# Optimization experiments

Hardware: AMD Instinct MI355X
Metric: run time of the kernel (lower is better)

Reference implementation:

```python
import jax, jax.numpy as jnp
import numpy as np

N = 100_000      # num_nodes
E = 1_600_000    # num_edges (avg degree 16)
D = 64           # embedding_dim
L = 3            # num_layers


def setup_inputs() -> dict:
    key = jax.random.key(0)
    k1, k2 = jax.random.split(key)
    edge_index = jax.random.randint(k1, (2, E), 0, N, dtype=jnp.int64)
    edge_weight = jnp.ones((E,), jnp.float32)
    # nn.init.normal_(std=0.1)
    embedding = 0.1 * jax.random.normal(k2, (N, D), dtype=jnp.float32)
    return {"embedding": embedding, "edge_weight": edge_weight, "edge_index": edge_index}


def reference(embedding, edge_weight, edge_index):
    n = embedding.shape[0]
    self_idx = jnp.arange(n, dtype=edge_index.dtype)
    # add_self_loops: append (i, i) with weight 1 (PyG default fill_value)
    row = jnp.concatenate([edge_index[0], self_idx])  # source j
    col = jnp.concatenate([edge_index[1], self_idx])  # target i
    ew = jnp.concatenate([edge_weight, jnp.ones((n,), embedding.dtype)])
    # degree() counts occurrences of row (unweighted)
    deg = jax.ops.segment_sum(jnp.ones_like(ew), row, num_segments=n)
    deg_inv_sqrt = jnp.where(deg > 0, jax.lax.rsqrt(deg), 0.0)
    norm = deg_inv_sqrt[row] * ew * deg_inv_sqrt[col]  # [E+N]

    x = embedding
    acc = embedding  # running sum of layer-0..L embeddings
    for _ in range(L):
        # gather from source, scale, scatter-add to target (dropout off in eval)
        msg = norm[:, None] * x[row]                       # [E+N, D]
        x = jax.ops.segment_sum(msg, col, num_segments=n)  # [N, D]
        acc = acc + x
    return acc / (L + 1)
```

## Files before the change

kernel.cpp:

```cpp
#include <hip/hip_runtime.h>
#include <stdint.h>

#define DIM 64
#define GB 256
#define GSH 8
#define CH 4096
#define TB1 256
#define HW 25000
#define NSL 256
#define TBH 1024

__device__ __forceinline__ unsigned bf16rne(float f) {
    unsigned u = __float_as_uint(f);
    return (u + 0x7FFFu + ((u >> 16) & 1u)) >> 16;
}
__device__ __forceinline__ unsigned pack2(float lo, float hi) {
    return bf16rne(lo) | (bf16rne(hi) << 16);
}
#define UNPK(u, lo, hi) { lo = __uint_as_float((u) << 16); hi = __uint_as_float((u) & 0xFFFF0000u); }

__global__ void __launch_bounds__(TBH)
hist_kernel(const int* __restrict__ src, const int* __restrict__ dst,
            unsigned* __restrict__ partials, int* __restrict__ bslice,
            int E, int N, int Es, int NB) {
    __shared__ unsigned h8[HW];
    __shared__ int hb[512];
    const int s = blockIdx.x;
    const int nw = (N + 3) >> 2;
    for (int j = threadIdx.x; j < nw; j += TBH) h8[j] = 0;
    for (int j = threadIdx.x; j < 512; j += TBH) hb[j] = 0;
    __syncthreads();
    const int e0 = s * Es, e1 = min(e0 + Es, E);
#pragma unroll 4
    for (int i = e0 + threadIdx.x; i < e1; i += TBH) {
        unsigned sj = (unsigned)src[i];
        unsigned tj = (unsigned)dst[i];
        atomicAdd(&h8[sj >> 2], 1u << ((sj & 3) * 8));
        atomicAdd(&hb[tj >> GSH], 1);
    }
    __syncthreads();
    unsigned* part = partials + (size_t)s * nw;
    for (int j = threadIdx.x; j < nw; j += TBH) part[j] = h8[j];
    for (int j = threadIdx.x; j < NB; j += TBH) bslice[s * 512 + j] = hb[j];
}

__global__ void __launch_bounds__(512)
merge_scan_kernel(const unsigned* __restrict__ partials, const int* __restrict__ bslice,
                  float* __restrict__ dis, int* __restrict__ bucket_base,
                  int* __restrict__ cursor, int* __restrict__ offsets,
                  int nw, int nmerge, int N, int NB) {
    __shared__ int buf[512];
    if ((int)blockIdx.x < nmerge) {
        const int w = blockIdx.x * 512 + threadIdx.x;
        if (w >= nw) return;
        int s0 = 0, s1 = 0, s2 = 0, s3 = 0;
#pragma unroll 8
        for (int s = 0; s < NSL; ++s) {
            unsigned v = partials[(size_t)s * nw + w];
            s0 += v & 255u; s1 += (v >> 8) & 255u;
            s2 += (v >> 16) & 255u; s3 += v >> 24;
        }
        const int nidx = w * 4;
        if (nidx + 3 < N) {
            *(float4*)(dis + nidx) = make_float4(
                rsqrtf((float)s0 + 1.f), rsqrtf((float)s1 + 1.f),
                rsqrtf((float)s2 + 1.f), rsqrtf((float)s3 + 1.f));
        } else {
            if (nidx + 0 < N) dis[nidx + 0] = rsqrtf((float)s0 + 1.f);
            if (nidx + 1 < N) dis[nidx + 1] = rsqrtf((float)s1 + 1.f);
            if (nidx + 2 < N) dis[nidx + 2] = rsqrtf((float)s2 + 1.f);
            if (nidx + 3 < N) dis[nidx + 3] = rsqrtf((float)s3 + 1.f);
        }
    } else {
        const int t = threadIdx.x;
        int v = 0;
        if (t < NB)
            for (int s = 0; s < NSL; ++s) v += bslice[s * 512 + t];
        buf[t] = v;
        __syncthreads();
        for (int off = 1; off < 512; off <<= 1) {
            int add = (t >= off) ? buf[t - off] : 0;
            __syncthreads();
            buf[t] += add;
            __syncthreads();
        }
        if (t < NB) { bucket_base[t] = buf[t] - v; cursor[t] = buf[t] - v; }
        if (t == NB - 1) { bucket_base[NB] = buf[t]; offsets[N] = buf[t]; }
    }
}

__global__ void __launch_bounds__(TB1)
part_conv_kernel(const int* __restrict__ src, const int* __restrict__ dst,
                 const float* __restrict__ ew,
                 int* __restrict__ cursor, int2* __restrict__ staged,
                 const float4* __restrict__ emb4, uint4* __restrict__ x0c,
                 int E, int NB, int npart, int n8) {
    __shared__ int h[512];
    if ((int)blockIdx.x >= npart) {
        const int i = (blockIdx.x - npart) * TB1 + threadIdx.x;
        if (i >= n8) return;
        float4 a = emb4[2 * i], b = emb4[2 * i + 1];
        uint4 o;
        o.x = pack2(a.x, a.y); o.y = pack2(a.z, a.w);
        o.z = pack2(b.x, b.y); o.w = pack2(b.z, b.w);
        x0c[i] = o;
        return;
    }
    const int tid = threadIdx.x;
    const int e0 = blockIdx.x * CH;
    const int e1 = min(e0 + CH, E);
    for (int j = tid; j < 512; j += TB1) h[j] = 0;
    __syncthreads();
    int4 d[CH / (TB1 * 4)];
    int ngrp = 0;
    for (int i = e0 + tid * 4, k = 0; i < e1; i += TB1 * 4, ++k) {
        int4 t;
        if (i + 3 < e1) t = *(const int4*)(dst + i);
        else {
            t.x = dst[i];
            t.y = (i + 1 < e1) ? dst[i + 1] : -1;
            t.z = (i + 2 < e1) ? dst[i + 2] : -1;
            t.w = (i + 3 < e1) ? dst[i + 3] : -1;
        }
        d[k] = t;
        if (t.x >= 0) atomicAdd(&h[t.x >> GSH], 1);
        if (t.y >= 0) atomicAdd(&h[t.y >> GSH], 1);
        if (t.z >= 0) atomicAdd(&h[t.z >> GSH], 1);
        if (t.w >= 0) atomicAdd(&h[t.w >> GSH], 1);
        ngrp = k + 1;
    }
    __syncthreads();
    for (int j = tid; j < NB; j += TB1) {
        int c = h[j];
        h[j] = c ? atomicAdd(&cursor[j], c) : 0;
    }
    __syncthreads();
    for (int i = e0 + tid * 4, k = 0; k < ngrp; i += TB1 * 4, ++k) {
        int4 t = d[k];
        int4 ss = make_int4(0, 0, 0, 0);
        float4 ww = make_float4(0.f, 0.f, 0.f, 0.f);
        if (i + 3 < e1) { ss = *(const int4*)(src + i); ww = *(const float4*)(ew + i); }
        else {
            ss.x = src[i]; ww.x = ew[i];
            if (i + 1 < e1) { ss.y = src[i + 1]; ww.y = ew[i + 1]; }
            if (i + 2 < e1) { ss.z = src[i + 2]; ww.z = ew[i + 2]; }
            if (i + 3 < e1) { ss.w = src[i + 3]; ww.w = ew[i + 3]; }
        }
#define PART1(T, S, W) if ((T) >= 0) { \
        int pos_ = atomicAdd(&h[(T) >> GSH], 1); \
        staged[pos_] = make_int2((S) | (((T) & (GB - 1)) << 20), __float_as_int(W)); }
        PART1(t.x, ss.x, ww.x)
        PART1(t.y, ss.y, ww.y)
        PART1(t.z, ss.z, ww.z)
        PART1(t.w, ss.w, ww.w)
#undef PART1
    }
}

__global__ void __launch_bounds__(256)
place_kernel(const int2* __restrict__ staged, const int* __restrict__ bucket_base,
             const float* __restrict__ dis,
             int* __restrict__ offsets, int2* __restrict__ csr, int N) {
    __shared__ int cnt[GB];
    __shared__ int cur[GB];
    __shared__ int pre[GB + 1];
    __shared__ float disb[GB];
    const int b = blockIdx.x;
    const int n0 = b << GSH;
    const int nb = min(GB, N - n0);
    const int r0 = bucket_base[b], r1 = bucket_base[b + 1];
    cnt[threadIdx.x] = 0;
    disb[threadIdx.x] = (threadIdx.x < nb) ? dis[n0 + threadIdx.x] : 0.f;
    __syncthreads();
    for (int i = r0 + threadIdx.x; i < r1; i += 256)
        atomicAdd(&cnt[(staged[i].x >> 20) & (GB - 1)], 1);
    __syncthreads();
    if (threadIdx.x == 0) {
        int run = r0;
        for (int j = 0; j < nb; ++j) { pre[j] = run; run += cnt[j]; }
        pre[nb] = run;
    }
    __syncthreads();
    if (threadIdx.x < nb) { offsets[n0 + threadIdx.x] = pre[threadIdx.x]; cur[threadIdx.x] = pre[threadIdx.x]; }
    __syncthreads();
    for (int i = r0 + threadIdx.x; i < r1; i += 256) {
        int2 rec = staged[i];
        int tl = (rec.x >> 20) & (GB - 1);
        int s = rec.x & 0xFFFFF;
        int rank = atomicAdd(&cur[tl], 1);
        float w = dis[s] * __int_as_float(rec.y) * disb[tl];
        csr[rank] = make_int2(s, __float_as_int(w));
    }
}

__global__ void __launch_bounds__(256)
prop_kernel(const uint4* __restrict__ xg, const float4* __restrict__ selfF,
            uint4* __restrict__ xstore,
            const int* __restrict__ offsets, const int2* __restrict__ csr,
            const float* __restrict__ dis, int n,
            const float4* __restrict__ embF, const uint4* __restrict__ xaF,
            float4* __restrict__ outF) {
    const int lane = threadIdx.x & 63;
    const int fl  = lane & 7;
    const int sub = lane >> 3;
    const int wave = blockIdx.x * (blockDim.x >> 6) + (threadIdx.x >> 6);
    const int node = wave * 8 + sub;
    if (node >= n) return;

    const int beg = offsets[node];
    const int end = offsets[node + 1];
    const float d = dis[node];
    const float dd = d * d;

    float a0, a1, a2, a3, a4, a5, a6, a7;
    uint4 qs = make_uint4(0, 0, 0, 0);
    if (selfF) {
        float4 s0 = selfF[(size_t)node * 16 + fl * 2];
        float4 s1 = selfF[(size_t)node * 16 + fl * 2 + 1];
        a0 = dd * s0.x; a1 = dd * s0.y; a2 = dd * s0.z; a3 = dd * s0.w;
        a4 = dd * s1.x; a5 = dd * s1.y; a6 = dd * s1.z; a7 = dd * s1.w;
    } else {
        qs = xg[(size_t)node * 8 + fl];
        float l, h;
        UNPK(qs.x, l, h) a0 = dd * l; a1 = dd * h;
        UNPK(qs.y, l, h) a2 = dd * l; a3 = dd * h;
        UNPK(qs.z, l, h) a4 = dd * l; a5 = dd * h;
        UNPK(qs.w, l, h) a6 = dd * l; a7 = dd * h;
    }

#define EDGE(E, Q) { float w_ = __int_as_float((E).y); float l, h; \
    UNPK((Q).x, l, h) a0 = fmaf(w_, l, a0); a1 = fmaf(w_, h, a1); \
    UNPK((Q).y, l, h) a2 = fmaf(w_, l, a2); a3 = fmaf(w_, h, a3); \
    UNPK((Q).z, l, h) a4 = fmaf(w_, l, a4); a5 = fmaf(w_, h, a5); \
    UNPK((Q).w, l, h) a6 = fmaf(w_, l, a6); a7 = fmaf(w_, h, a7); }

    int p = beg;
    for (; p + 8 <= end; p += 8) {
        int2 e0 = csr[p + 0], e1 = csr[p + 1], e2 = csr[p + 2], e3 = csr[p + 3];
        int2 e4 = csr[p + 4], e5 = csr[p + 5], e6 = csr[p + 6], e7 = csr[p + 7];
        uint4 q0 = xg[(size_t)e0.x * 8 + fl];
        uint4 q1 = xg[(size_t)e1.x * 8 + fl];
        uint4 q2 = xg[(size_t)e2.x * 8 + fl];
        uint4 q3 = xg[(size_t)e3.x * 8 + fl];
        uint4 q4 = xg[(size_t)e4.x * 8 + fl];
        uint4 q5 = xg[(size_t)e5.x * 8 + fl];
        uint4 q6 = xg[(size_t)e6.x * 8 + fl];
        uint4 q7 = xg[(size_t)e7.x * 8 + fl];
        EDGE(e0, q0) EDGE(e1, q1) EDGE(e2, q2) EDGE(e3, q3)
        EDGE(e4, q4) EDGE(e5, q5) EDGE(e6, q6) EDGE(e7, q7)
    }
    for (; p + 4 <= end; p += 4) {
        int2 e0 = csr[p + 0], e1 = csr[p + 1], e2 = csr[p + 2], e3 = csr[p + 3];
        uint4 q0 = xg[(size_t)e0.x * 8 + fl];
        uint4 q1 = xg[(size_t)e1.x * 8 + fl];
        uint4 q2 = xg[(size_t)e2.x * 8 + fl];
        uint4 q3 = xg[(size_t)e3.x * 8 + fl];
        EDGE(e0, q0) EDGE(e1, q1) EDGE(e2, q2) EDGE(e3, q3)
    }
    for (; p < end; ++p) {
        int2 e = csr[p];
        uint4 q = xg[(size_t)e.x * 8 + fl];
        EDGE(e, q)
    }
#undef EDGE

    if (outF) {
        float4 eA = embF[(size_t)node * 16 + fl * 2];
        float4 eB = embF[(size_t)node * 16 + fl * 2 + 1];
        uint4 qa = xaF[(size_t)node * 8 + fl];
        float r0 = eA.x + a0, r1 = eA.y + a1, r2 = eA.z + a2, r3 = eA.w + a3;
        float r4 = eB.x + a4, r5 = eB.y + a5, r6 = eB.z + a6, r7 = eB.w + a7;
        float l, h;
        UNPK(qa.x, l, h) r0 += l; r1 += h;
        UNPK(qa.y, l, h) r2 += l; r3 += h;
        UNPK(qa.z, l, h) r4 += l; r5 += h;
        UNPK(qa.w, l, h) r6 += l; r7 += h;
        UNPK(qs.x, l, h) r0 += l; r1 += h;
        UNPK(qs.y, l, h) r2 += l; r3 += h;
        UNPK(qs.z, l, h) r4 += l; r5 += h;
        UNPK(qs.w, l, h) r6 += l; r7 += h;
        outF[(size_t)node * 16 + fl * 2] =
            make_float4(0.25f * r0, 0.25f * r1, 0.25f * r2, 0.25f * r3);
        outF[(size_t)node * 16 + fl * 2 + 1] =
            make_float4(0.25f * r4, 0.25f * r5, 0.25f * r6, 0.25f * r7);
    } else {
        uint4 o;
        o.x = pack2(a0, a1); o.y = pack2(a2, a3);
        o.z = pack2(a4, a5); o.w = pack2(a6, a7);
        xstore[(size_t)node * 8 + fl] = o;
    }
}


extern "C" void kernel_launch(void* const* d_in, const int* in_sizes, int n_in,
                              void* d_out, int out_size, void* d_ws, size_t ws_size,
                              hipStream_t stream) {
    const float* emb = (const float*)d_in[0];
    const float* ew  = (const float*)d_in[1];
    const int*   ei  = (const int*)d_in[2];
    const int E = in_sizes[2] / 2;
    const int N = in_sizes[0] / DIM;
    const int* src = ei;
    const int* dst = ei + E;
    float* out = (float*)d_out;

    const int NB = (N + GB - 1) >> GSH;
    const int Es = (E + NSL - 1) / NSL;
    const int nw = (N + 3) >> 2;

    char* w = (char*)d_ws;
    size_t xSz = ((size_t)N * DIM * 2 + 255) & ~(size_t)255;
    size_t sSz = ((size_t)E * 8 + 255) & ~(size_t)255;
    size_t pSz = ((size_t)NSL * nw * 4 + 255) & ~(size_t)255;
    size_t uSz = xSz > sSz ? xSz : sSz; if (pSz > uSz) uSz = pSz;
    unsigned* partials = (unsigned*)w;
    int2* staged = (int2*)w;
    uint4* xb    = (uint4*)w; w += uSz;
    int2* csr    = (int2*)w; w += sSz;
    uint4* x0c   = (uint4*)w; w += xSz;
    uint4* xa    = (uint4*)w; w += xSz;
    int* offsets = (int*)w; w += ((size_t)(N + 1) * 4 + 255) & ~(size_t)255;
    float* dis   = (float*)w; w += ((size_t)N * 4 + 255) & ~(size_t)255;
    int* bslice      = (int*)w; w += (size_t)NSL * 512 * 4;
    int* bucket_base = (int*)w; w += 513 * 4;
    int* cursor      = (int*)w; w += 512 * 4;

    const int TB = 256;

    hist_kernel<<<NSL, TBH, 0, stream>>>(src, dst, partials, bslice, E, N, Es, NB);

    const int nmerge = (nw + 511) / 512;
    merge_scan_kernel<<<nmerge + 1, 512, 0, stream>>>(partials, bslice, dis,
                                                      bucket_base, cursor, offsets,
                                                      nw, nmerge, N, NB);

    const int n8 = N * DIM / 8;
    const int npart = (E + CH - 1) / CH;
    const int nconv = (n8 + TB - 1) / TB;
    part_conv_kernel<<<npart + nconv, TB1, 0, stream>>>(src, dst, ew, cursor, staged,
                                                        (const float4*)emb, x0c,
                                                        E, NB, npart, n8);
    place_kernel<<<NB, TB, 0, stream>>>(staged, bucket_base, dis, offsets, csr, N);

    dim3 grid((N + 31) / 32), block(TB);
    prop_kernel<<<grid, block, 0, stream>>>(x0c, (const float4*)emb, xa,
                                            offsets, csr, dis, N,
                                            nullptr, nullptr, nullptr);
    prop_kernel<<<grid, block, 0, stream>>>(xa, nullptr, xb,
                                            offsets, csr, dis, N,
                                            nullptr, nullptr, nullptr);
    prop_kernel<<<grid, block, 0, stream>>>(xb, nullptr, nullptr,
                                            offsets, csr, dis, N,
                                            (const float4*)emb, xa, (float4*)out);
}
```

Before: 263.1 us.

## Split bucket scan into single-block kernel, fold degree merge into partition kernel

The degree-merge work (summing per-slice histograms into rsqrt degrees) moves out of the merge/scan kernel and into extra blocks of the partition/convert kernel, leaving a tiny single-block scan kernel. The aim is to shorten the serial critical path so the merge overlaps with partitioning, which also forces the workspace to be re-aliased so partials and staged edges do not clash. The propagation kernels now write their outputs with nontemporal stores to reduce cache pollution. This adds aliasing risk and more blocks in the partition launch.

```diff
diff --git a/kernel.cpp b/kernel.cpp
--- a/kernel.cpp
+++ b/kernel.cpp
@@ -18,6 +18,17 @@
     return bf16rne(lo) | (bf16rne(hi) << 16);
 }
 #define UNPK(u, lo, hi) { lo = __uint_as_float((u) << 16); hi = __uint_as_float((u) & 0xFFFF0000u); }
+
+typedef unsigned uv4_t __attribute__((ext_vector_type(4)));
+typedef float    fv4_t __attribute__((ext_vector_type(4)));
+__device__ __forceinline__ void ntstore_u4(uint4* p, uint4 q) {
+    uv4_t v = { q.x, q.y, q.z, q.w };
+    __builtin_nontemporal_store(v, (uv4_t*)p);
+}
+__device__ __forceinline__ void ntstore_f4(float4* p, float4 q) {
+    fv4_t v = { q.x, q.y, q.z, q.w };
+    __builtin_nontemporal_store(v, (fv4_t*)p);
+}
 
 __global__ void __launch_bounds__(TBH)
 hist_kernel(const int* __restrict__ src, const int* __restrict__ dst,
@@ -45,13 +56,36 @@
 }
 
 __global__ void __launch_bounds__(512)
-merge_scan_kernel(const unsigned* __restrict__ partials, const int* __restrict__ bslice,
-                  float* __restrict__ dis, int* __restrict__ bucket_base,
-                  int* __restrict__ cursor, int* __restrict__ offsets,
-                  int nw, int nmerge, int N, int NB) {
+scan_buckets(const int* __restrict__ bslice, int* __restrict__ bucket_base,
+             int* __restrict__ cursor, int* __restrict__ offsets, int NB, int N) {
     __shared__ int buf[512];
-    if ((int)blockIdx.x < nmerge) {
-        const int w = blockIdx.x * 512 + threadIdx.x;
+    const int t = threadIdx.x;
+    int v = 0;
+    if (t < NB)
+        for (int s = 0; s < NSL; ++s) v += bslice[s * 512 + t];
+    buf[t] = v;
+    __syncthreads();
+    for (int off = 1; off < 512; off <<= 1) {
+        int add = (t >= off) ? buf[t - off] : 0;
+        __syncthreads();
+        buf[t] += add;
+        __syncthreads();
+    }
+    if (t < NB) { bucket_base[t] = buf[t] - v; cursor[t] = buf[t] - v; }
+    if (t == NB - 1) { bucket_base[NB] = buf[t]; offsets[N] = buf[t]; }
+}
+
+__global__ void __launch_bounds__(TB1)
+part_conv_kernel(const int* __restrict__ src, const int* __restrict__ dst,
+                 const float* __restrict__ ew,
+                 int* __restrict__ cursor, int2* __restrict__ staged,
+                 const float4* __restrict__ emb4, uint4* __restrict__ x0c,
+                 const unsigned* __restrict__ partials, float* __restrict__ dis,
+                 int E, int NB, int npart, int nconv, int n8, int nw, int N) {
+    __shared__ int h[512];
+    const int bid = blockIdx.x;
+    if (bid >= npart + nconv) {
+        const int w = (bid - npart - nconv) * TB1 + threadIdx.x;
         if (w >= nw) return;
         int s0 = 0, s1 = 0, s2 = 0, s3 = 0;
 #pragma unroll 8
@@ -71,33 +105,10 @@
             if (nidx + 2 < N) dis[nidx + 2] = rsqrtf((float)s2 + 1.f);
             if (nidx + 3 < N) dis[nidx + 3] = rsqrtf((float)s3 + 1.f);
         }
-    } else {
-        const int t = threadIdx.x;
-        int v = 0;
-        if (t < NB)
-            for (int s = 0; s < NSL; ++s) v += bslice[s * 512 + t];
-        buf[t] = v;
-        __syncthreads();
-        for (int off = 1; off < 512; off <<= 1) {
-            int add = (t >= off) ? buf[t - off] : 0;
-            __syncthreads();
-            buf[t] += add;
-            __syncthreads();
-        }
-        if (t < NB) { bucket_base[t] = buf[t] - v; cursor[t] = buf[t] - v; }
-        if (t == NB - 1) { bucket_base[NB] = buf[t]; offsets[N] = buf[t]; }
-    }
-}
-
-__global__ void __launch_bounds__(TB1)
-part_conv_kernel(const int* __restrict__ src, const int* __restrict__ dst,
-                 const float* __restrict__ ew,
-                 int* __restrict__ cursor, int2* __restrict__ staged,
-                 const float4* __restrict__ emb4, uint4* __restrict__ x0c,
-                 int E, int NB, int npart, int n8) {
-    __shared__ int h[512];
-    if ((int)blockIdx.x >= npart) {
-        const int i = (blockIdx.x - npart) * TB1 + threadIdx.x;
+        return;
+    }
+    if (bid >= npart) {
+        const int i = (bid - npart) * TB1 + threadIdx.x;
         if (i >= n8) return;
         float4 a = emb4[2 * i], b = emb4[2 * i + 1];
         uint4 o;
@@ -107,7 +118,7 @@
         return;
     }
     const int tid = threadIdx.x;
-    const int e0 = blockIdx.x * CH;
+    const int e0 = bid * CH;
     const int e1 = min(e0 + CH, E);
     for (int j = tid; j < 512; j += TB1) h[j] = 0;
     __syncthreads();
@@ -279,15 +290,15 @@
         UNPK(qs.y, l, h) r2 += l; r3 += h;
         UNPK(qs.z, l, h) r4 += l; r5 += h;
         UNPK(qs.w, l, h) r6 += l; r7 += h;
-        outF[(size_t)node * 16 + fl * 2] =
-            make_float4(0.25f * r0, 0.25f * r1, 0.25f * r2, 0.25f * r3);
-        outF[(size_t)node * 16 + fl * 2 + 1] =
-            make_float4(0.25f * r4, 0.25f * r5, 0.25f * r6, 0.25f * r7);
+        ntstore_f4(&outF[(size_t)node * 16 + fl * 2],
+                   make_float4(0.25f * r0, 0.25f * r1, 0.25f * r2, 0.25f * r3));
+        ntstore_f4(&outF[(size_t)node * 16 + fl * 2 + 1],
+                   make_float4(0.25f * r4, 0.25f * r5, 0.25f * r6, 0.25f * r7));
     } else {
         uint4 o;
         o.x = pack2(a0, a1); o.y = pack2(a2, a3);
         o.z = pack2(a4, a5); o.w = pack2(a6, a7);
-        xstore[(size_t)node * 8 + fl] = o;
+        ntstore_u4(&xstore[(size_t)node * 8 + fl], o);
     }
 }
 
@@ -312,37 +323,33 @@
     size_t xSz = ((size_t)N * DIM * 2 + 255) & ~(size_t)255;
     size_t sSz = ((size_t)E * 8 + 255) & ~(size_t)255;
     size_t pSz = ((size_t)NSL * nw * 4 + 255) & ~(size_t)255;
-    size_t uSz = xSz > sSz ? xSz : sSz; if (pSz > uSz) uSz = pSz;
+    size_t u1 = pSz > xSz ? pSz : xSz;
+    size_t u2 = sSz > xSz ? sSz : xSz;
     unsigned* partials = (unsigned*)w;
+    uint4* xb    = (uint4*)w; w += u1;
     int2* staged = (int2*)w;
-    uint4* xb    = (uint4*)w; w += uSz;
+    uint4* xa    = (uint4*)w; w += u2;
     int2* csr    = (int2*)w; w += sSz;
     uint4* x0c   = (uint4*)w; w += xSz;
-    uint4* xa    = (uint4*)w; w += xSz;
     int* offsets = (int*)w; w += ((size_t)(N + 1) * 4 + 255) & ~(size_t)255;
     float* dis   = (float*)w; w += ((size_t)N * 4 + 255) & ~(size_t)255;
     int* bslice      = (int*)w; w += (size_t)NSL * 512 * 4;
     int* bucket_base = (int*)w; w += 513 * 4;
     int* cursor      = (int*)w; w += 512 * 4;
 
-    const int TB = 256;
-
     hist_kernel<<<NSL, TBH, 0, stream>>>(src, dst, partials, bslice, E, N, Es, NB);
-
-    const int nmerge = (nw + 511) / 512;
-    merge_scan_kernel<<<nmerge + 1, 512, 0, stream>>>(partials, bslice, dis,
-                                                      bucket_base, cursor, offsets,
-                                                      nw, nmerge, N, NB);
+    scan_buckets<<<1, 512, 0, stream>>>(bslice, bucket_base, cursor, offsets, NB, N);
 
     const int n8 = N * DIM / 8;
     const int npart = (E + CH - 1) / CH;
-    const int nconv = (n8 + TB - 1) / TB;
-    part_conv_kernel<<<npart + nconv, TB1, 0, stream>>>(src, dst, ew, cursor, staged,
-                                                        (const float4*)emb, x0c,
-                                                        E, NB, npart, n8);
-    place_kernel<<<NB, TB, 0, stream>>>(staged, bucket_base, dis, offsets, csr, N);
-
-    dim3 grid((N + 31) / 32), block(TB);
+    const int nconv = (n8 + TB1 - 1) / TB1;
+    const int nmerge = (nw + TB1 - 1) / TB1;
+    part_conv_kernel<<<npart + nconv + nmerge, TB1, 0, stream>>>(
+        src, dst, ew, cursor, staged, (const float4*)emb, x0c,
+        partials, dis, E, NB, npart, nconv, n8, nw, N);
+    place_kernel<<<NB, 256, 0, stream>>>(staged, bucket_base, dis, offsets, csr, N);
+
+    dim3 grid((N + 31) / 32), block(256);
     prop_kernel<<<grid, block, 0, stream>>>(x0c, (const float4*)emb, xa,
                                             offsets, csr, dis, N,
                                             nullptr, nullptr, nullptr);
```

Result: no change. 264.3 us (+0.4%).
